# Kernel optimization log

Measured on AMD Instinct MI355X. Metric: run time of the kernel, lower is better.

Reference implementation:

```python
import jax, jax.numpy as jnp
import numpy as np

CH = 256  # channels

def setup_inputs() -> dict:
    key = jax.random.key(0)
    ks = jax.random.split(key, 9)
    B, H, W = 8, 64, 64
    c8, c2 = CH // 8, CH // 2
    s = lambda fan_in: 1.0 / np.sqrt(fan_in)
    return {
        "x": jax.random.normal(ks[0], (B, H, W, CH), dtype=jnp.float32),
        "Wq": jax.random.normal(ks[1], (CH, c8), dtype=jnp.float32) * s(CH),
        "bq": jnp.zeros((c8,), dtype=jnp.float32),
        "Wk": jax.random.normal(ks[2], (CH, c8), dtype=jnp.float32) * s(CH),
        "bk": jnp.zeros((c8,), dtype=jnp.float32),
        "Wv": jax.random.normal(ks[3], (CH, c2), dtype=jnp.float32) * s(CH),
        "bv": jnp.zeros((c2,), dtype=jnp.float32),
        "Wo": jax.random.normal(ks[4], (c2, CH), dtype=jnp.float32) * s(c2),
        "bo": jnp.zeros((CH,), dtype=jnp.float32),
    }

def reference(x, Wq, bq, Wk, bk, Wv, bv, Wo, bo):
    B, H, W, C = x.shape
    # 1x1 convs are per-pixel matmuls over the channel dim
    q = x @ Wq + bq                      # [B,H,W,C/8]
    k = x @ Wk + bk                      # [B,H,W,C/8]
    v = x @ Wv + bv                      # [B,H,W,C/2]
    N = H * W
    qf = q.reshape(B, N, -1)
    kf = k.reshape(B, N, -1)
    vf = v.reshape(B, N, -1)
    # full self-attention over flattened spatial positions (no scaling, per source)
    scores = jnp.einsum('bnd,bmd->bnm', qf, kf)   # [B,N,N]
    attn = jax.nn.softmax(scores, axis=-1)
    out = jnp.einsum('bnm,bmd->bnd', attn, vf)    # [B,N,C/2]
    out = out.reshape(B, H, W, -1)
    return out @ Wo + bo + x
```

## Files before the change

kernel.cpp:

```cpp
#include <hip/hip_runtime.h>

typedef __attribute__((ext_vector_type(8))) short short8;
typedef __attribute__((ext_vector_type(4))) float f32x4;
typedef __attribute__((ext_vector_type(16))) float f32x16;

__device__ __forceinline__ unsigned short f2bf(float f) {
  unsigned int u = __float_as_uint(f);
  u += 0x7fffu + ((u >> 16) & 1u);
  return (unsigned short)(u >> 16);
}
__device__ __forceinline__ float bf2f(unsigned short h) {
  return __uint_as_float(((unsigned int)h) << 16);
}
__device__ __forceinline__ unsigned int pkbf(float a, float b) {
  return (unsigned int)f2bf(a) | ((unsigned int)f2bf(b) << 16);
}
__device__ __forceinline__ short8 ld8(const unsigned short* p) {
  return *(const short8*)p;
}
__device__ __forceinline__ int swap23(int x) {
  return (x & 0x13) | ((x & 4) << 1) | ((x & 8) >> 1);
}
#define MFMA(a, b, c) __builtin_amdgcn_mfma_f32_16x16x32_bf16((a), (b), (c), 0, 0, 0)
#define MFMA32(a, b, c) __builtin_amdgcn_mfma_f32_32x32x16_bf16((a), (b), (c), 0, 0, 0)
#define LOG2E 1.4426950408889634f
#define MCONST 96.0f

__global__ void prep_weights(const float* __restrict__ Wq, const float* __restrict__ Wk,
                             const float* __restrict__ Wv, const float* __restrict__ Wo,
                             unsigned short* __restrict__ Wth, unsigned short* __restrict__ Wtl,
                             unsigned short* __restrict__ WoT) {
  int idx = blockIdx.x * 256 + threadIdx.x;
  if (idx < 192 * 256) {
    int o = idx >> 8, c = idx & 255;
    float w = (o < 32) ? Wq[c * 32 + o] : (o < 64) ? Wk[c * 32 + (o - 32)] : Wv[c * 128 + (o - 64)];
    unsigned short h = f2bf(w);
    Wth[idx] = h;
    Wtl[idx] = f2bf(w - bf2f(h));
  } else if (idx < 192 * 256 + 256 * 128) {
    int j = idx - 192 * 256;
    int c = j >> 7, d = j & 127;
    WoT[j] = f2bf(Wo[d * 256 + c]);
  }
}

__global__ __launch_bounds__(256) void proj_qkv(
    const float* __restrict__ x,
    const unsigned short* __restrict__ Wth, const unsigned short* __restrict__ Wtl,
    const float* __restrict__ bq, const float* __restrict__ bk, const float* __restrict__ bv,
    unsigned short* __restrict__ qh, unsigned short* __restrict__ qlo,
    unsigned short* __restrict__ khF, unsigned short* __restrict__ klF,
    unsigned short* __restrict__ VF) {
  __shared__ unsigned short xsh[32][264];
  __shared__ unsigned short xsl[32][264];
  __shared__ unsigned short st[8192];
  const int pix0 = blockIdx.x * 32;
  const int b = pix0 >> 12;
  const int nloc0 = pix0 & 4095;
  const int tid = threadIdx.x;

#pragma unroll
  for (int i = 0; i < 8; ++i) {
    int chunk = i * 256 + tid;
    int row = chunk >> 6;
    int c4 = (chunk & 63) * 4;
    float4 v = *(const float4*)(x + (size_t)(pix0 + row) * 256 + c4);
    unsigned short h0 = f2bf(v.x), h1 = f2bf(v.y), h2 = f2bf(v.z), h3 = f2bf(v.w);
    unsigned short l0 = f2bf(v.x - bf2f(h0)), l1 = f2bf(v.y - bf2f(h1));
    unsigned short l2 = f2bf(v.z - bf2f(h2)), l3 = f2bf(v.w - bf2f(h3));
    uint2 hp, lp;
    hp.x = (unsigned int)h0 | ((unsigned int)h1 << 16);
    hp.y = (unsigned int)h2 | ((unsigned int)h3 << 16);
    lp.x = (unsigned int)l0 | ((unsigned int)l1 << 16);
    lp.y = (unsigned int)l2 | ((unsigned int)l3 << 16);
    *(uint2*)&xsh[row][c4] = hp;
    *(uint2*)&xsl[row][c4] = lp;
  }
  __syncthreads();

  const int wave = tid >> 6, lane = tid & 63, l = lane & 15, qd = lane >> 4;
#pragma unroll
  for (int si = 0; si < 3; ++si) {
    const int sub = wave + si * 4;
    const int outc0 = sub * 16;
    if (si == 0) {
      const int outc = outc0 + l;
      const float bias = (outc < 32) ? bq[outc] : bk[outc - 32];
      f32x4 acc[2];
      acc[0] = (f32x4){bias, bias, bias, bias};
      acc[1] = (f32x4){bias, bias, bias, bias};
#pragma unroll
      for (int kc = 0; kc < 8; ++kc) {
        short8 whf = ld8(Wth + (size_t)(outc0 + l) * 256 + kc * 32 + qd * 8);
        short8 wlf = ld8(Wtl + (size_t)(outc0 + l) * 256 + kc * 32 + qd * 8);
#pragma unroll
        for (int m = 0; m < 2; ++m) {
          short8 xhf = ld8(&xsh[m * 16 + l][kc * 32 + qd * 8]);
          short8 xlf = ld8(&xsl[m * 16 + l][kc * 32 + qd * 8]);
          acc[m] = MFMA(xlf, whf, acc[m]);
          acc[m] = MFMA(xhf, wlf, acc[m]);
          acc[m] = MFMA(xhf, whf, acc[m]);
        }
      }
      if (wave < 2) {
#pragma unroll
        for (int m = 0; m < 2; ++m)
#pragma unroll
          for (int r = 0; r < 4; ++r) {
            const int p = m * 16 + 4 * qd + r;
            float val = acc[m][r] * LOG2E;
            unsigned short h = f2bf(val);
            st[p * 32 + outc] = h;
            st[1024 + p * 32 + outc] = f2bf(val - bf2f(h));
          }
      } else {
        const int kd = outc - 32;
        const int step = kd >> 4, hh = (kd >> 3) & 1, e = kd & 7;
#pragma unroll
        for (int m = 0; m < 2; ++m)
#pragma unroll
          for (int r = 0; r < 4; ++r) {
            const int p = m * 16 + 4 * qd + r;
            const int addr = 2048 + step * 512 + (hh * 32 + swap23(p)) * 8 + e;
            float val = acc[m][r];
            unsigned short h = f2bf(val);
            st[addr] = h;
            st[addr + 1024] = f2bf(val - bf2f(h));
          }
      }
    } else {
      const int dv0 = outc0 - 64;
      const float b0 = bv[dv0 + 4 * qd + 0], b1 = bv[dv0 + 4 * qd + 1];
      const float b2 = bv[dv0 + 4 * qd + 2], b3 = bv[dv0 + 4 * qd + 3];
      f32x4 acc[2];
      acc[0] = (f32x4){b0, b1, b2, b3};
      acc[1] = (f32x4){b0, b1, b2, b3};
#pragma unroll
      for (int kc = 0; kc < 8; ++kc) {
        short8 whf = ld8(Wth + (size_t)(outc0 + l) * 256 + kc * 32 + qd * 8);
#pragma unroll
        for (int m = 0; m < 2; ++m) {
          short8 xhf = ld8(&xsh[m * 16 + l][kc * 32 + qd * 8]);
          acc[m] = MFMA(whf, xhf, acc[m]);
        }
      }
#pragma unroll
      for (int m = 0; m < 2; ++m)
#pragma unroll
        for (int r = 0; r < 4; ++r) {
          const int dv = dv0 + 4 * qd + r;
          const int dt = dv >> 5, lam = dv & 31;
          const int p = m * 16 + l;
          const int ks = p >> 4, hh = (p >> 3) & 1, e = p & 7;
          st[4096 + ((dt * 2 + ks) * 64 + hh * 32 + lam) * 8 + e] = f2bf(acc[m][r]);
        }
    }
  }
  __syncthreads();

  const int nt_ = nloc0 >> 6;
  const int kt_ = (nloc0 >> 5) & 1;
  const uint4* stv = (const uint4*)st;
#pragma unroll
  for (int i = 0; i < 4; ++i) {
    const int flat = i * 256 + tid;
    const uint4 val = stv[flat];
    if (flat < 128) {
      ((uint4*)(qh + (size_t)pix0 * 32))[flat] = val;
    } else if (flat < 256) {
      ((uint4*)(qlo + (size_t)pix0 * 32))[flat - 128] = val;
    } else if (flat < 384) {
      ((uint4*)(khF + ((size_t)(b * 64 + nt_) * 2 + kt_) * 1024))[flat - 256] = val;
    } else if (flat < 512) {
      ((uint4*)(klF + ((size_t)(b * 64 + nt_) * 2 + kt_) * 1024))[flat - 384] = val;
    } else {
      const int v = flat - 512;
      const int dt = v >> 7, ks = (v >> 6) & 1, off = v & 63;
      ((uint4*)(VF + ((size_t)(b * 64 + nt_) * 16 + dt * 4 + kt_ * 2 + ks) * 512))[off] = val;
    }
  }
}

__global__ __launch_bounds__(256) void flash_attn(
    const unsigned short* __restrict__ qh, const unsigned short* __restrict__ qlo,
    const unsigned short* __restrict__ khF, const unsigned short* __restrict__ klF,
    const unsigned short* __restrict__ VF, unsigned short* __restrict__ opart,
    float* __restrict__ lstat) {
  const int b = blockIdx.x & 7;
  const int r6 = blockIdx.x >> 3;
  const int tile = r6 & 15;
  const int split = r6 >> 4;
  const int wave = threadIdx.x >> 6;
  const int lane = threadIdx.x & 63;
  const int lam = lane & 31;
  const int h = lane >> 5;
  const int m0 = tile * 256 + wave * 64;

  const unsigned short* qh_b = qh + (size_t)b * 4096 * 32;
  const unsigned short* ql_b = qlo + (size_t)b * 4096 * 32;

  short8 qhf[2][2], qlf[2][2];
#pragma unroll
  for (int set = 0; set < 2; ++set)
#pragma unroll
    for (int step = 0; step < 2; ++step) {
      size_t off = (size_t)(m0 + set * 32 + lam) * 32 + step * 16 + h * 8;
      qhf[set][step] = ld8(qh_b + off);
      qlf[set][step] = ld8(ql_b + off);
    }

  f32x16 acc[2][4];
#pragma unroll
  for (int set = 0; set < 2; ++set)
#pragma unroll
    for (int dt = 0; dt < 4; ++dt)
#pragma unroll
      for (int e = 0; e < 16; ++e) acc[set][dt][e] = 0.f;
  float lrun[2] = {0.f, 0.f};

#pragma unroll 1
  for (int it = 0; it < 16; ++it) {
    const int nt = split * 16 + it;
    const unsigned short* kb = khF + (size_t)(b * 64 + nt) * 2048;
    const unsigned short* lb = klF + (size_t)(b * 64 + nt) * 2048;
    const unsigned short* vb = VF + (size_t)(b * 64 + nt) * 8192;

    short8 kf_h[2][2], kf_l[2][2];
#pragma unroll
    for (int kt = 0; kt < 2; ++kt)
#pragma unroll
      for (int step = 0; step < 2; ++step) {
        kf_h[kt][step] = ld8(kb + (kt * 2 + step) * 512 + lane * 8);
        kf_l[kt][step] = ld8(lb + (kt * 2 + step) * 512 + lane * 8);
      }
    short8 vf[4][4];
#pragma unroll
    for (int dt = 0; dt < 4; ++dt)
#pragma unroll
      for (int ks = 0; ks < 4; ++ks)
        vf[dt][ks] = ld8(vb + (dt * 4 + ks) * 512 + lane * 8);

    unsigned int pp[2][2][8];
#pragma unroll
    for (int kt = 0; kt < 2; ++kt)
#pragma unroll
      for (int set = 0; set < 2; ++set) {
        f32x16 z;
#pragma unroll
        for (int e = 0; e < 16; ++e) z[e] = 0.f;
#pragma unroll
        for (int step = 0; step < 2; ++step) {
          z = MFMA32(kf_l[kt][step], qhf[set][step], z);
          z = MFMA32(kf_h[kt][step], qlf[set][step], z);
          z = MFMA32(kf_h[kt][step], qhf[set][step], z);
        }
        float ls = 0.f;
#pragma unroll
        for (int g = 0; g < 8; ++g) {
          float p0 = __builtin_amdgcn_exp2f(z[2 * g] - MCONST);
          float p1 = __builtin_amdgcn_exp2f(z[2 * g + 1] - MCONST);
          ls += p0 + p1;
          pp[set][kt][g] = pkbf(p0, p1);
        }
        lrun[set] += ls;
      }

#pragma unroll
    for (int dt = 0; dt < 4; ++dt) {
#pragma unroll
      for (int ks = 0; ks < 4; ++ks) {
        union { unsigned int u[4]; short8 v; } pfA, pfB;
#pragma unroll
        for (int d = 0; d < 4; ++d) {
          pfA.u[d] = pp[0][ks >> 1][4 * (ks & 1) + d];
          pfB.u[d] = pp[1][ks >> 1][4 * (ks & 1) + d];
        }
        acc[0][dt] = MFMA32(vf[dt][ks], pfA.v, acc[0][dt]);
        acc[1][dt] = MFMA32(vf[dt][ks], pfB.v, acc[1][dt]);
      }
    }
  }

#pragma unroll
  for (int set = 0; set < 2; ++set) {
    const float ltot = lrun[set] + __shfl_xor(lrun[set], 32);
    const int grow = b * 4096 + m0 + set * 32 + lam;
    if (h == 0) lstat[split * 32768 + grow] = ltot;
    const size_t obase = ((size_t)split * 32768 + grow) * 128;
#pragma unroll
    for (int dt = 0; dt < 4; ++dt)
#pragma unroll
      for (int g = 0; g < 8; ++g) {
        int r = 2 * g;
        int dv = dt * 32 + (r & 3) + 8 * (r >> 2) + 4 * h;
        *(unsigned int*)(opart + obase + dv) = pkbf(acc[set][dt][r], acc[set][dt][r + 1]);
      }
  }
}

__global__ __launch_bounds__(256) void combine_splits(
    const unsigned short* __restrict__ opart, const float* __restrict__ lstat,
    unsigned short* __restrict__ ao) {
  const int tid = threadIdx.x;
  const int row = blockIdx.x * 16 + (tid >> 4);
  const int col = (tid & 15) * 8;
  float den = lstat[row] + lstat[32768 + row] + lstat[65536 + row] + lstat[98304 + row];
  float inv = 1.f / den;
  float o[8] = {0.f, 0.f, 0.f, 0.f, 0.f, 0.f, 0.f, 0.f};
#pragma unroll
  for (int s = 0; s < 4; ++s) {
    uint4 v = *(const uint4*)(opart + ((size_t)s * 32768 + row) * 128 + col);
    unsigned int uu[4] = {v.x, v.y, v.z, v.w};
#pragma unroll
    for (int j = 0; j < 4; ++j) {
      o[2 * j]     += bf2f((unsigned short)(uu[j] & 0xffff));
      o[2 * j + 1] += bf2f((unsigned short)(uu[j] >> 16));
    }
  }
  uint4 outv;
  outv.x = pkbf(o[0] * inv, o[1] * inv);
  outv.y = pkbf(o[2] * inv, o[3] * inv);
  outv.z = pkbf(o[4] * inv, o[5] * inv);
  outv.w = pkbf(o[6] * inv, o[7] * inv);
  *(uint4*)(ao + (size_t)row * 128 + col) = outv;
}

__global__ __launch_bounds__(256) void out_proj(
    const unsigned short* __restrict__ ao, const unsigned short* __restrict__ WoT,
    const float* __restrict__ bo, const float* __restrict__ x, float* __restrict__ out) {
  const int pix0 = blockIdx.x * 64;
  const int wave = threadIdx.x >> 6, lane = threadIdx.x & 63, l = lane & 15, qd = lane >> 4;
  const int base = pix0 + wave * 16;
  short8 af[4];
#pragma unroll
  for (int kc = 0; kc < 4; ++kc)
    af[kc] = ld8(ao + (size_t)(base + l) * 128 + kc * 32 + qd * 8);
#pragma unroll
  for (int sub = 0; sub < 16; ++sub) {
    const int c = sub * 16 + l;
    const float bias = bo[c];
    f32x4 acc = (f32x4){bias, bias, bias, bias};
#pragma unroll
    for (int kc = 0; kc < 4; ++kc) {
      short8 wf = ld8(WoT + (size_t)c * 128 + kc * 32 + qd * 8);
      acc = MFMA(af[kc], wf, acc);
    }
#pragma unroll
    for (int r = 0; r < 4; ++r) {
      const size_t pixel = (size_t)base + 4 * qd + r;
      out[pixel * 256 + c] = acc[r] + x[pixel * 256 + c];
    }
  }
}

extern "C" void kernel_launch(void* const* d_in, const int* in_sizes, int n_in,
                              void* d_out, int out_size, void* d_ws, size_t ws_size,
                              hipStream_t stream) {
  const float* x  = (const float*)d_in[0];
  const float* Wq = (const float*)d_in[1];
  const float* bq = (const float*)d_in[2];
  const float* Wk = (const float*)d_in[3];
  const float* bk = (const float*)d_in[4];
  const float* Wv = (const float*)d_in[5];
  const float* bv = (const float*)d_in[6];
  const float* Wo = (const float*)d_in[7];
  const float* bo = (const float*)d_in[8];

  char* ws = (char*)d_ws;
  unsigned short* qh  = (unsigned short*)(ws + 0);
  unsigned short* qlo = (unsigned short*)(ws + 2097152);
  unsigned short* khF = (unsigned short*)(ws + 4194304);
  unsigned short* klF = (unsigned short*)(ws + 6291456);
  unsigned short* VF  = (unsigned short*)(ws + 8388608);
  unsigned short* ao  = (unsigned short*)(ws + 16777216);
  unsigned short* Wth = (unsigned short*)(ws + 25165824);
  unsigned short* Wtl = (unsigned short*)(ws + 25264128);
  unsigned short* WoT = (unsigned short*)(ws + 25362432);
  float*          lst = (float*)(ws + 25493504);
  unsigned short* opart = (unsigned short*)d_out;

  prep_weights<<<320, 256, 0, stream>>>(Wq, Wk, Wv, Wo, Wth, Wtl, WoT);
  proj_qkv<<<1024, 256, 0, stream>>>(x, Wth, Wtl, bq, bk, bv, qh, qlo, khF, klF, VF);
  flash_attn<<<512, 256, 0, stream>>>(qh, qlo, khF, klF, VF, opart, lst);
  combine_splits<<<2048, 256, 0, stream>>>(opart, lst, ao);
  out_proj<<<512, 256, 0, stream>>>(ao, WoT, bo, x, (float*)d_out);
}
```

Measured before the change: 221.8 us.

## Stage K/V tiles through double-buffered LDS with register prefetch in flash attention

Each of the four waves previously loaded the full K-hi, K-lo and V tiles from global memory on its own. Now the block loads each tile cooperatively, one quarter per wave, into a double-buffered shared-memory buffer, and prefetches the tile two iterations ahead into registers. The aim is to cut redundant global and L2 traffic by four and hide load latency behind the MFMA work. In exchange it adds two block barriers per iteration and 48 KB of LDS per block, which may reduce occupancy.

```diff
diff --git a/kernel.cpp b/kernel.cpp
--- a/kernel.cpp
+++ b/kernel.cpp
@@ -25,6 +25,7 @@
 #define MFMA32(a, b, c) __builtin_amdgcn_mfma_f32_32x32x16_bf16((a), (b), (c), 0, 0, 0)
 #define LOG2E 1.4426950408889634f
 #define MCONST 96.0f
+#define LGKM_BARRIER() asm volatile("s_waitcnt lgkmcnt(0)\n\ts_barrier" ::: "memory")
 
 __global__ void prep_weights(const float* __restrict__ Wq, const float* __restrict__ Wk,
                              const float* __restrict__ Wv, const float* __restrict__ Wo,
@@ -186,6 +187,7 @@
     const unsigned short* __restrict__ khF, const unsigned short* __restrict__ klF,
     const unsigned short* __restrict__ VF, unsigned short* __restrict__ opart,
     float* __restrict__ lstat) {
+  __shared__ unsigned short sbuf[2][12288];
   const int b = blockIdx.x & 7;
   const int r6 = blockIdx.x >> 3;
   const int tile = r6 & 15;
@@ -199,6 +201,13 @@
   const unsigned short* qh_b = qh + (size_t)b * 4096 * 32;
   const unsigned short* ql_b = qlo + (size_t)b * 4096 * 32;
 
+  auto fsrc = [&](int f, int nt) -> const unsigned short* {
+    const size_t t = (size_t)(b * 64 + nt);
+    if (f < 4) return khF + t * 2048 + f * 512 + lane * 8;
+    if (f < 8) return klF + t * 2048 + (f - 4) * 512 + lane * 8;
+    return VF + t * 8192 + (f - 8) * 512 + lane * 8;
+  };
+
   short8 qhf[2][2], qlf[2][2];
 #pragma unroll
   for (int set = 0; set < 2; ++set)
@@ -218,27 +227,33 @@
       for (int e = 0; e < 16; ++e) acc[set][dt][e] = 0.f;
   float lrun[2] = {0.f, 0.f};
 
+  short8 stg[6];
+  {
+    const int nt0 = split * 16;
+    short8 t0[6];
+#pragma unroll
+    for (int j = 0; j < 6; ++j) t0[j] = ld8(fsrc(j * 4 + wave, nt0));
+#pragma unroll
+    for (int j = 0; j < 6; ++j)
+      *(short8*)&sbuf[0][(j * 4 + wave) * 512 + lane * 8] = t0[j];
+#pragma unroll
+    for (int j = 0; j < 6; ++j) stg[j] = ld8(fsrc(j * 4 + wave, nt0 + 1));
+    LGKM_BARRIER();
+  }
+
 #pragma unroll 1
   for (int it = 0; it < 16; ++it) {
-    const int nt = split * 16 + it;
-    const unsigned short* kb = khF + (size_t)(b * 64 + nt) * 2048;
-    const unsigned short* lb = klF + (size_t)(b * 64 + nt) * 2048;
-    const unsigned short* vb = VF + (size_t)(b * 64 + nt) * 8192;
+    const int cur = it & 1;
+    const unsigned short* sb = sbuf[cur];
 
     short8 kf_h[2][2], kf_l[2][2];
 #pragma unroll
     for (int kt = 0; kt < 2; ++kt)
 #pragma unroll
       for (int step = 0; step < 2; ++step) {
-        kf_h[kt][step] = ld8(kb + (kt * 2 + step) * 512 + lane * 8);
-        kf_l[kt][step] = ld8(lb + (kt * 2 + step) * 512 + lane * 8);
-      }
-    short8 vf[4][4];
-#pragma unroll
-    for (int dt = 0; dt < 4; ++dt)
-#pragma unroll
-      for (int ks = 0; ks < 4; ++ks)
-        vf[dt][ks] = ld8(vb + (dt * 4 + ks) * 512 + lane * 8);
+        kf_h[kt][step] = *(const short8*)&sb[(kt * 2 + step) * 512 + lane * 8];
+        kf_l[kt][step] = *(const short8*)&sb[(4 + kt * 2 + step) * 512 + lane * 8];
+      }
 
     unsigned int pp[2][2][8];
 #pragma unroll
@@ -269,15 +284,30 @@
     for (int dt = 0; dt < 4; ++dt) {
 #pragma unroll
       for (int ks = 0; ks < 4; ++ks) {
+        short8 vfr = *(const short8*)&sb[(8 + dt * 4 + ks) * 512 + lane * 8];
         union { unsigned int u[4]; short8 v; } pfA, pfB;
 #pragma unroll
         for (int d = 0; d < 4; ++d) {
           pfA.u[d] = pp[0][ks >> 1][4 * (ks & 1) + d];
           pfB.u[d] = pp[1][ks >> 1][4 * (ks & 1) + d];
         }
-        acc[0][dt] = MFMA32(vf[dt][ks], pfA.v, acc[0][dt]);
-        acc[1][dt] = MFMA32(vf[dt][ks], pfB.v, acc[1][dt]);
-      }
+        acc[0][dt] = MFMA32(vfr, pfA.v, acc[0][dt]);
+        acc[1][dt] = MFMA32(vfr, pfB.v, acc[1][dt]);
+      }
+    }
+
+    LGKM_BARRIER();
+
+    if (it < 15) {
+#pragma unroll
+      for (int j = 0; j < 6; ++j)
+        *(short8*)&sbuf[cur ^ 1][(j * 4 + wave) * 512 + lane * 8] = stg[j];
+      if (it < 14) {
+#pragma unroll
+        for (int j = 0; j < 6; ++j)
+          stg[j] = ld8(fsrc(j * 4 + wave, split * 16 + it + 2));
+      }
+      LGKM_BARRIER();
     }
   }
 
```

Measured after the change: 227.1 us. +2.4%, slower.
